# Performance work log

Hardware: AMD Instinct MI355X
Metric: run time of the kernel (lower is better)

## Reference

```python
import jax, jax.numpy as jnp
import numpy as np

HEAD = 4

def setup_inputs() -> dict:
    key = jax.random.key(0)
    ks = jax.random.split(key, 6)
    b, h, w, dim, attn_dim = 2, 64, 64, 256, 128
    return {
        "query": jax.random.normal(ks[0], (b, h, w, dim), jnp.float32),
        "context": jax.random.normal(ks[1], (b, h, w, dim), jnp.float32),
        "Wq": jax.random.normal(ks[2], (dim, attn_dim), jnp.float32) * (dim ** -0.5),
        "Wk": jax.random.normal(ks[3], (dim, attn_dim), jnp.float32) * (dim ** -0.5),
        "Wv": jax.random.normal(ks[4], (dim, attn_dim), jnp.float32) * (dim ** -0.5),
        "Wo": jax.random.normal(ks[5], (attn_dim, dim), jnp.float32) * (attn_dim ** -0.5),
    }

def reference(query, context, Wq, Wk, Wv, Wo):
    b, h, w, c = query.shape
    attn_dim = Wq.shape[1]
    head = HEAD
    head_dim = attn_dim // head
    scale = head_dim ** -0.5
    n = h * w
    # 1x1 conv, no bias == per-pixel dense projection
    q = (query.reshape(b, n, c) @ Wq).reshape(b, n, head, head_dim)
    k = (context.reshape(b, n, c) @ Wk).reshape(b, n, head, head_dim)
    v = (context.reshape(b, n, c) @ Wv).reshape(b, n, head, head_dim)
    score = jnp.einsum('bihd,bjhd->bijh', q, k) * scale  # [b, n, n, head]
    attn = jax.nn.softmax(score, axis=-2)  # softmax over key axis j
    out = jnp.einsum('bijh,bjhd->bihd', attn, v).reshape(b, n, attn_dim)
    return (out @ Wo).reshape(b, h, w, c)
```

## Files before the change

### kernel.cpp

```cpp
#include <hip/hip_runtime.h>
#include <hip/hip_bf16.h>
#include <math.h>

#define N_TOK 4096
#define C_DIM 256
#define A_DIM 128
#define HEADS 4
#define HD    32
#define NBAT  2
#define BH    (NBAT * HEADS)

#define SCALE_LOG2E 0.25503521f

#define SPLITS 8
#define KEYS_PER_SPLIT (N_TOK / SPLITS)

#define KS 40
#define VS 72
#define PS 40

typedef __attribute__((ext_vector_type(8))) short short8;
typedef __attribute__((ext_vector_type(4))) short short4_t;
typedef __attribute__((ext_vector_type(4))) float floatx4;
typedef __attribute__((ext_vector_type(2))) unsigned int uint2v;

__device__ __forceinline__ unsigned short f2bf(float f) {
    unsigned int u = __float_as_uint(f);
    u = (u + 0x7fffu + ((u >> 16) & 1u)) >> 16;
    return (unsigned short)u;
}
__device__ __forceinline__ float bf2f(unsigned short u) {
    return __uint_as_float((unsigned int)u << 16);
}
__device__ __forceinline__ unsigned int pack2(float a, float b) {
    unsigned int lo = (__float_as_uint(a) + 0x8000u) >> 16;
    unsigned int hi = (__float_as_uint(b) + 0x8000u) & 0xffff0000u;
    return hi | lo;
}

__global__ __launch_bounds__(256) void wpack_kernel(
    const float* __restrict__ Wq, const float* __restrict__ Wk,
    const float* __restrict__ Wv, const float* __restrict__ Wo,
    unsigned short* __restrict__ Wp)
{
    const int chunk = blockIdx.x * 256 + threadIdx.x;
    const int wid = chunk >> 12;
    const int c = chunk & 4095;
    const int lane = c & 63, quad = lane >> 4, l15 = lane & 15;
    short8 v;
    if (wid < 3) {
        const int s = c >> 9, t = (c >> 6) & 7;
        const float* W = (wid == 0) ? Wq : ((wid == 1) ? Wk : Wv);
        const float scale = (wid == 0) ? SCALE_LOG2E : 1.0f;
        const int src = (s * 32 + quad * 8) * A_DIM + t * 16 + l15;
        #pragma unroll
        for (int j = 0; j < 8; j++) v[j] = (short)f2bf(W[src + j * A_DIM] * scale);
    } else {
        const int s = c >> 10, t = (c >> 6) & 15;
        const int src = (s * 32 + quad * 8) * C_DIM + t * 16 + l15;
        #pragma unroll
        for (int j = 0; j < 8; j++) v[j] = (short)f2bf(Wo[src + j * C_DIM]);
    }
    *(short8*)(Wp + (long)chunk * 8) = v;
}

__global__ __launch_bounds__(256) void qkv_kernel(
    const float* __restrict__ query, const float* __restrict__ context,
    const unsigned short* __restrict__ Wp,
    unsigned short* __restrict__ Qb, unsigned short* __restrict__ Kb,
    unsigned short* __restrict__ Vb)
{
    __shared__ __align__(16) unsigned short V_lds[128 * 18];

    const int tid = threadIdx.x;
    const int w = tid >> 6, lane = tid & 63;
    const int quad = lane >> 4, l15 = lane & 15;
    const int ch = w;
    const long i0 = (long)blockIdx.x * 16;
    const long row = i0 + l15;

    const unsigned short* Wqp = Wp;
    const unsigned short* Wkp = Wp + 32768;
    const unsigned short* Wvp = Wp + 65536;

    floatx4 aQ[2] = {}, aK[2] = {}, aV[2] = {};

    for (int s = 0; s < 8; s++) {
        const float* qp = query + row * C_DIM + s * 32 + quad * 8;
        const float* cp = context + row * C_DIM + s * 32 + quad * 8;
        floatx4 q0 = *(const floatx4*)qp, q1 = *(const floatx4*)(qp + 4);
        floatx4 c0 = *(const floatx4*)cp, c1 = *(const floatx4*)(cp + 4);
        short8 aq, ac;
        #pragma unroll
        for (int j = 0; j < 4; j++) {
            aq[j] = (short)f2bf(q0[j]); aq[4 + j] = (short)f2bf(q1[j]);
            ac[j] = (short)f2bf(c0[j]); ac[4 + j] = (short)f2bf(c1[j]);
        }
        #pragma unroll
        for (int tp = 0; tp < 2; tp++) {
            const long fo = ((long)(s * 8 + ch * 2 + tp) * 64 + lane) * 8;
            short8 bq = *(const short8*)(Wqp + fo);
            short8 bk = *(const short8*)(Wkp + fo);
            short8 bv = *(const short8*)(Wvp + fo);
            aQ[tp] = __builtin_amdgcn_mfma_f32_16x16x32_bf16(aq, bq, aQ[tp], 0, 0, 0);
            aK[tp] = __builtin_amdgcn_mfma_f32_16x16x32_bf16(ac, bk, aK[tp], 0, 0, 0);
            aV[tp] = __builtin_amdgcn_mfma_f32_16x16x32_bf16(ac, bv, aV[tp], 0, 0, 0);
        }
    }

    const long b = i0 >> 12;
    const long n0 = i0 & (N_TOK - 1);
    const long nbase = n0 + quad * 4;
    #pragma unroll
    for (int tp = 0; tp < 2; tp++) {
        const int col = ch * 32 + tp * 16 + l15;
        const int h = col >> 5, d = col & 31;
        unsigned short* qdst = Qb + ((b * HEADS + h) * N_TOK + nbase) * HD + d;
        unsigned short* kdst = Kb + ((b * HEADS + h) * N_TOK + nbase) * HD + d;
        #pragma unroll
        for (int r = 0; r < 4; r++) {
            qdst[r * HD] = f2bf(aQ[tp][r]);
            kdst[r * HD] = f2bf(aK[tp][r]);
        }
        short4_t pv;
        #pragma unroll
        for (int r = 0; r < 4; r++) pv[r] = (short)f2bf(aV[tp][r]);
        *(short4_t*)&V_lds[col * 18 + quad * 4] = pv;
    }
    __syncthreads();

    {
        const int col = tid >> 1, seg = tid & 1;
        const int h = col >> 5, d = col & 31;
        unsigned short* dst = Vb + ((b * HEADS + h) * HD + d) * N_TOK + n0 + seg * 8;
        *(short8*)dst = *(const short8*)&V_lds[col * 18 + seg * 8];
    }
}

__global__ __launch_bounds__(256, 2) void attn_kernel(
    const unsigned short* __restrict__ Qb, const unsigned short* __restrict__ Kb,
    const unsigned short* __restrict__ Vb,
    unsigned short* __restrict__ AO, float* __restrict__ Lbuf)
{
    __shared__ __align__(16) unsigned short K_lds[64 * KS];
    __shared__ __align__(16) unsigned short V_lds[HD * VS];
    __shared__ __align__(16) unsigned short P_lds[4][64 * PS];

    const int tid  = threadIdx.x;
    const int w    = tid >> 6;
    const int lane = tid & 63;
    const int quad = lane >> 4;
    const int l15  = lane & 15;

    const int L  = blockIdx.x;
    const int qb = (L >> 3) & 15;
    const int g  = (L & 7) + 8 * (L >> 7);
    const int bh = g & 7;
    const int z  = g >> 3;
    const int i0 = qb * 256 + w * 64;

    const unsigned short* Qh = Qb + (long)bh * N_TOK * HD;
    const unsigned short* Kh = Kb + (long)bh * N_TOK * HD;
    const unsigned short* Vh = Vb + (long)bh * HD * N_TOK;

    short8 qf[4];
    #pragma unroll
    for (int t = 0; t < 4; t++)
        qf[t] = *(const short8*)(Qh + (long)(i0 + t * 16 + l15) * HD + quad * 8);

    floatx4 acc[4][2] = {};
    float lc[4] = {0.f, 0.f, 0.f, 0.f};

    const int  kst = (tid >> 2) * KS + (tid & 3) * 8;
    const int  vst = (tid >> 3) * VS + (tid & 7) * 8;
    const long vgl = (long)(tid >> 3) * N_TOK + (tid & 7) * 8;
    unsigned int* Pq = (unsigned int*)&P_lds[w][0];

    const int j_lo = z * KEYS_PER_SPLIT, j_hi = j_lo + KEYS_PER_SPLIT;

    short8 kreg = *(const short8*)(Kh + (long)j_lo * HD + tid * 8);
    short8 vreg = *(const short8*)(Vh + vgl + j_lo);

    for (int j0 = j_lo; j0 < j_hi; j0 += 64) {
        __syncthreads();
        *(short8*)&K_lds[kst] = kreg;
        *(short8*)&V_lds[vst] = vreg;
        if (j0 + 64 < j_hi) {
            kreg = *(const short8*)(Kh + (long)(j0 + 64) * HD + tid * 8);
            vreg = *(const short8*)(Vh + vgl + j0 + 64);
        }
        __syncthreads();

        #pragma unroll
        for (int sub = 0; sub < 2; sub++) {
            const int jb = sub * 32;
            const floatx4 zf = {0.f,0.f,0.f,0.f};

            {
                short8 kf = *(short8*)&K_lds[(jb + l15) * KS + quad * 8];
                #pragma unroll
                for (int t = 0; t < 4; t++) {
                    floatx4 s = __builtin_amdgcn_mfma_f32_16x16x32_bf16(kf, qf[t], zf, 0, 0, 0);
                    float p0 = __builtin_amdgcn_exp2f(s[0]);
                    float p1 = __builtin_amdgcn_exp2f(s[1]);
                    float p2 = __builtin_amdgcn_exp2f(s[2]);
                    float p3 = __builtin_amdgcn_exp2f(s[3]);
                    lc[t] += (p0 + p1) + (p2 + p3);
                    uint2v pk; pk[0] = pack2(p0, p1); pk[1] = pack2(p2, p3);
                    *(uint2v*)&Pq[(t * 16 + l15) * 20 + quad * 2] = pk;
                }
            }
            {
                short8 kf = *(short8*)&K_lds[(jb + 16 + l15) * KS + quad * 8];
                #pragma unroll
                for (int t = 0; t < 4; t++) {
                    floatx4 s = __builtin_amdgcn_mfma_f32_16x16x32_bf16(kf, qf[t], zf, 0, 0, 0);
                    float p0 = __builtin_amdgcn_exp2f(s[0]);
                    float p1 = __builtin_amdgcn_exp2f(s[1]);
                    float p2 = __builtin_amdgcn_exp2f(s[2]);
                    float p3 = __builtin_amdgcn_exp2f(s[3]);
                    lc[t] += (p0 + p1) + (p2 + p3);
                    uint2v pk; pk[0] = pack2(p0, p1); pk[1] = pack2(p2, p3);
                    *(uint2v*)&Pq[(t * 16 + l15) * 20 + 8 + quad * 2] = pk;
                }
            }

            short8 vf0 = *(short8*)&V_lds[l15 * VS + jb + quad * 8];
            short8 vf1 = *(short8*)&V_lds[(16 + l15) * VS + jb + quad * 8];
            #pragma unroll
            for (int t = 0; t < 4; t++) {
                short8 pf = *(short8*)&P_lds[w][(t * 16 + l15) * PS + quad * 8];
                acc[t][0] = __builtin_amdgcn_mfma_f32_16x16x32_bf16(pf, vf0, acc[t][0], 0, 0, 0);
                acc[t][1] = __builtin_amdgcn_mfma_f32_16x16x32_bf16(pf, vf1, acc[t][1], 0, 0, 0);
            }
        }
    }

    #pragma unroll
    for (int t = 0; t < 4; t++) {
        lc[t] += __shfl_xor(lc[t], 16);
        lc[t] += __shfl_xor(lc[t], 32);
    }

    const int b = bh >> 2, h = bh & 3;
    unsigned short* AOz = AO + (long)z * (NBAT * N_TOK * A_DIM);
    float* Lz = Lbuf + (long)z * (BH * N_TOK);
    if (quad == 0) {
        #pragma unroll
        for (int t = 0; t < 4; t++)
            Lz[(long)bh * N_TOK + i0 + t * 16 + l15] = lc[t];
    }
    #pragma unroll
    for (int t = 0; t < 4; t++) {
        #pragma unroll
        for (int r = 0; r < 4; r++) {
            const float inv = 1.0f / __shfl(lc[t], quad * 4 + r);
            const long row = (long)b * N_TOK + i0 + t * 16 + quad * 4 + r;
            AOz[row * A_DIM + h * HD + l15]      = f2bf(acc[t][0][r] * inv);
            AOz[row * A_DIM + h * HD + 16 + l15] = f2bf(acc[t][1][r] * inv);
        }
    }
}

__global__ __launch_bounds__(256) void outproj_kernel(
    const unsigned short* __restrict__ AO, const float* __restrict__ Lbuf,
    const unsigned short* __restrict__ Wp, float* __restrict__ out)
{
    const int tid = threadIdx.x;
    const int w = tid >> 6, lane = tid & 63;
    const int quad = lane >> 4, l15 = lane & 15;
    const int ch = w;
    const long i0 = (long)blockIdx.x * 16;
    const long row = i0 + l15;
    const int b = (int)(row >> 12);
    const int n = (int)(row & (N_TOK - 1));
    const unsigned short* Wop = Wp + 98304;

    floatx4 acc[4] = {};

    #pragma unroll
    for (int s = 0; s < 4; s++) {
        float lz[SPLITS], lsum = 0.f;
        #pragma unroll
        for (int z = 0; z < SPLITS; z++) {
            lz[z] = Lbuf[(long)z * (BH * N_TOK) + (long)(b * HEADS + s) * N_TOK + n];
            lsum += lz[z];
        }
        const float inv = 1.0f / lsum;
        float vals[8] = {};
        #pragma unroll
        for (int z = 0; z < SPLITS; z++) {
            short8 az = *(const short8*)(AO + (long)z * (NBAT * N_TOK * A_DIM) +
                                         row * A_DIM + s * 32 + quad * 8);
            const float wz = lz[z] * inv;
            #pragma unroll
            for (int j = 0; j < 8; j++) vals[j] += wz * bf2f((unsigned short)az[j]);
        }
        short8 af;
        #pragma unroll
        for (int j = 0; j < 8; j++) af[j] = (short)f2bf(vals[j]);
        #pragma unroll
        for (int tp = 0; tp < 4; tp++) {
            const int t = ch * 4 + tp;
            short8 bo = *(const short8*)(Wop + ((long)(s * 16 + t) * 64 + lane) * 8);
            acc[tp] = __builtin_amdgcn_mfma_f32_16x16x32_bf16(af, bo, acc[tp], 0, 0, 0);
        }
    }

    #pragma unroll
    for (int tp = 0; tp < 4; tp++) {
        #pragma unroll
        for (int r = 0; r < 4; r++)
            out[(i0 + quad * 4 + r) * C_DIM + (ch * 4 + tp) * 16 + l15] = acc[tp][r];
    }
}

extern "C" void kernel_launch(void* const* d_in, const int* in_sizes, int n_in,
                              void* d_out, int out_size, void* d_ws, size_t ws_size,
                              hipStream_t stream)
{
    const float* query   = (const float*)d_in[0];
    const float* context = (const float*)d_in[1];
    const float* Wq      = (const float*)d_in[2];
    const float* Wk      = (const float*)d_in[3];
    const float* Wv      = (const float*)d_in[4];
    const float* Wo      = (const float*)d_in[5];
    float* out = (float*)d_out;

    char* ws = (char*)d_ws;
    unsigned short* Qb = (unsigned short*)(ws);
    unsigned short* Kb = (unsigned short*)(ws + (2 << 20));
    unsigned short* Vb = (unsigned short*)(ws + (4 << 20));
    unsigned short* AO = (unsigned short*)(ws + (6 << 20));
    float*          Lb = (float*)(ws + (22 << 20));
    unsigned short* Wp = (unsigned short*)(ws + (23 << 20));

    wpack_kernel<<<dim3(64), dim3(256), 0, stream>>>(Wq, Wk, Wv, Wo, Wp);
    qkv_kernel<<<dim3(512), dim3(256), 0, stream>>>(query, context, Wp, Qb, Kb, Vb);
    attn_kernel<<<dim3(16 * BH * SPLITS), dim3(256), 0, stream>>>(
        Qb, Kb, Vb, AO, Lb);
    outproj_kernel<<<dim3(512), dim3(256), 0, stream>>>(AO, Lb, Wp, out);
}
```

Before: 127.9 us.

## Load K/V MFMA fragments directly from global memory, dropping LDS staging

The attention kernel no longer stages K and V tiles through shared memory with two block-wide barriers per 64-key step. Each wave now loads its K and V MFMA operand fragments straight from global memory (expected to hit L2/L1), with a 2x unrolled 32-key loop. This removes the barriers and LDS traffic, at the cost of four waves redundantly fetching the same K/V and exposing global-load latency without explicit prefetch. Separately, f2bf switches from round-to-nearest-even to simpler round-half-up.

```diff
diff --git a/kernel.cpp b/kernel.cpp
--- a/kernel.cpp
+++ b/kernel.cpp
@@ -15,8 +15,6 @@
 #define SPLITS 8
 #define KEYS_PER_SPLIT (N_TOK / SPLITS)
 
-#define KS 40
-#define VS 72
 #define PS 40
 
 typedef __attribute__((ext_vector_type(8))) short short8;
@@ -25,9 +23,7 @@
 typedef __attribute__((ext_vector_type(2))) unsigned int uint2v;
 
 __device__ __forceinline__ unsigned short f2bf(float f) {
-    unsigned int u = __float_as_uint(f);
-    u = (u + 0x7fffu + ((u >> 16) & 1u)) >> 16;
-    return (unsigned short)u;
+    return (unsigned short)((__float_as_uint(f) + 0x8000u) >> 16);
 }
 __device__ __forceinline__ float bf2f(unsigned short u) {
     return __uint_as_float((unsigned int)u << 16);
@@ -142,8 +138,6 @@
     const unsigned short* __restrict__ Vb,
     unsigned short* __restrict__ AO, float* __restrict__ Lbuf)
 {
-    __shared__ __align__(16) unsigned short K_lds[64 * KS];
-    __shared__ __align__(16) unsigned short V_lds[HD * VS];
     __shared__ __align__(16) unsigned short P_lds[4][64 * PS];
 
     const int tid  = threadIdx.x;
@@ -171,68 +165,51 @@
     floatx4 acc[4][2] = {};
     float lc[4] = {0.f, 0.f, 0.f, 0.f};
 
-    const int  kst = (tid >> 2) * KS + (tid & 3) * 8;
-    const int  vst = (tid >> 3) * VS + (tid & 7) * 8;
-    const long vgl = (long)(tid >> 3) * N_TOK + (tid & 7) * 8;
     unsigned int* Pq = (unsigned int*)&P_lds[w][0];
 
+    const unsigned short* kp0 = Kh + (long)l15 * HD + quad * 8;
+    const unsigned short* kp1 = Kh + (long)(16 + l15) * HD + quad * 8;
+    const unsigned short* vp0 = Vh + (long)l15 * N_TOK + quad * 8;
+    const unsigned short* vp1 = Vh + (long)(16 + l15) * N_TOK + quad * 8;
+
     const int j_lo = z * KEYS_PER_SPLIT, j_hi = j_lo + KEYS_PER_SPLIT;
 
-    short8 kreg = *(const short8*)(Kh + (long)j_lo * HD + tid * 8);
-    short8 vreg = *(const short8*)(Vh + vgl + j_lo);
-
-    for (int j0 = j_lo; j0 < j_hi; j0 += 64) {
-        __syncthreads();
-        *(short8*)&K_lds[kst] = kreg;
-        *(short8*)&V_lds[vst] = vreg;
-        if (j0 + 64 < j_hi) {
-            kreg = *(const short8*)(Kh + (long)(j0 + 64) * HD + tid * 8);
-            vreg = *(const short8*)(Vh + vgl + j0 + 64);
-        }
-        __syncthreads();
-
-        #pragma unroll
-        for (int sub = 0; sub < 2; sub++) {
-            const int jb = sub * 32;
-            const floatx4 zf = {0.f,0.f,0.f,0.f};
-
-            {
-                short8 kf = *(short8*)&K_lds[(jb + l15) * KS + quad * 8];
-                #pragma unroll
-                for (int t = 0; t < 4; t++) {
-                    floatx4 s = __builtin_amdgcn_mfma_f32_16x16x32_bf16(kf, qf[t], zf, 0, 0, 0);
-                    float p0 = __builtin_amdgcn_exp2f(s[0]);
-                    float p1 = __builtin_amdgcn_exp2f(s[1]);
-                    float p2 = __builtin_amdgcn_exp2f(s[2]);
-                    float p3 = __builtin_amdgcn_exp2f(s[3]);
-                    lc[t] += (p0 + p1) + (p2 + p3);
-                    uint2v pk; pk[0] = pack2(p0, p1); pk[1] = pack2(p2, p3);
-                    *(uint2v*)&Pq[(t * 16 + l15) * 20 + quad * 2] = pk;
-                }
-            }
-            {
-                short8 kf = *(short8*)&K_lds[(jb + 16 + l15) * KS + quad * 8];
-                #pragma unroll
-                for (int t = 0; t < 4; t++) {
-                    floatx4 s = __builtin_amdgcn_mfma_f32_16x16x32_bf16(kf, qf[t], zf, 0, 0, 0);
-                    float p0 = __builtin_amdgcn_exp2f(s[0]);
-                    float p1 = __builtin_amdgcn_exp2f(s[1]);
-                    float p2 = __builtin_amdgcn_exp2f(s[2]);
-                    float p3 = __builtin_amdgcn_exp2f(s[3]);
-                    lc[t] += (p0 + p1) + (p2 + p3);
-                    uint2v pk; pk[0] = pack2(p0, p1); pk[1] = pack2(p2, p3);
-                    *(uint2v*)&Pq[(t * 16 + l15) * 20 + 8 + quad * 2] = pk;
-                }
-            }
-
-            short8 vf0 = *(short8*)&V_lds[l15 * VS + jb + quad * 8];
-            short8 vf1 = *(short8*)&V_lds[(16 + l15) * VS + jb + quad * 8];
-            #pragma unroll
-            for (int t = 0; t < 4; t++) {
-                short8 pf = *(short8*)&P_lds[w][(t * 16 + l15) * PS + quad * 8];
-                acc[t][0] = __builtin_amdgcn_mfma_f32_16x16x32_bf16(pf, vf0, acc[t][0], 0, 0, 0);
-                acc[t][1] = __builtin_amdgcn_mfma_f32_16x16x32_bf16(pf, vf1, acc[t][1], 0, 0, 0);
-            }
+    #pragma unroll 2
+    for (int j0 = j_lo; j0 < j_hi; j0 += 32) {
+        const floatx4 zf = {0.f,0.f,0.f,0.f};
+        short8 kf0 = *(const short8*)(kp0 + (long)j0 * HD);
+        short8 kf1 = *(const short8*)(kp1 + (long)j0 * HD);
+        short8 vf0 = *(const short8*)(vp0 + j0);
+        short8 vf1 = *(const short8*)(vp1 + j0);
+
+        #pragma unroll
+        for (int t = 0; t < 4; t++) {
+            floatx4 s = __builtin_amdgcn_mfma_f32_16x16x32_bf16(kf0, qf[t], zf, 0, 0, 0);
+            float p0 = __builtin_amdgcn_exp2f(s[0]);
+            float p1 = __builtin_amdgcn_exp2f(s[1]);
+            float p2 = __builtin_amdgcn_exp2f(s[2]);
+            float p3 = __builtin_amdgcn_exp2f(s[3]);
+            lc[t] += (p0 + p1) + (p2 + p3);
+            uint2v pk; pk[0] = pack2(p0, p1); pk[1] = pack2(p2, p3);
+            *(uint2v*)&Pq[(t * 16 + l15) * 20 + quad * 2] = pk;
+        }
+        #pragma unroll
+        for (int t = 0; t < 4; t++) {
+            floatx4 s = __builtin_amdgcn_mfma_f32_16x16x32_bf16(kf1, qf[t], zf, 0, 0, 0);
+            float p0 = __builtin_amdgcn_exp2f(s[0]);
+            float p1 = __builtin_amdgcn_exp2f(s[1]);
+            float p2 = __builtin_amdgcn_exp2f(s[2]);
+            float p3 = __builtin_amdgcn_exp2f(s[3]);
+            lc[t] += (p0 + p1) + (p2 + p3);
+            uint2v pk; pk[0] = pack2(p0, p1); pk[1] = pack2(p2, p3);
+            *(uint2v*)&Pq[(t * 16 + l15) * 20 + 8 + quad * 2] = pk;
+        }
+
+        #pragma unroll
+        for (int t = 0; t < 4; t++) {
+            short8 pf = *(short8*)&P_lds[w][(t * 16 + l15) * PS + quad * 8];
+            acc[t][0] = __builtin_amdgcn_mfma_f32_16x16x32_bf16(pf, vf0, acc[t][0], 0, 0, 0);
+            acc[t][1] = __builtin_amdgcn_mfma_f32_16x16x32_bf16(pf, vf1, acc[t][1], 0, 0, 0);
         }
     }
 
```

Result: no change. 128.8 us (+0.7%).
